# Performance work log

Measured on AMD Instinct MI355X. Metric: run time of the kernel, lower is better.

## Reference

```python
import jax, jax.numpy as jnp
import numpy as np
import math

B, L, H, U = 4, 4096, 1024, 1024


def setup_inputs() -> dict:
    key = jax.random.key(0)
    k_in, k_wi, k_bi, k_wo, k_bo, k_u = jax.random.split(key, 6)
    inputs = jax.random.normal(k_in, (B, L, H), dtype=jnp.float32)
    # Linear layers (torch Linear: y = x @ W.T + b), scaled like torch default init
    Wi = jax.random.normal(k_wi, (U, H), dtype=jnp.float32) / math.sqrt(H)
    bi = jax.random.normal(k_bi, (U,), dtype=jnp.float32) * 0.01
    Wo = jax.random.normal(k_wo, (H, U), dtype=jnp.float32) / math.sqrt(U)
    bo = jax.random.normal(k_bo, (H,), dtype=jnp.float32) * 0.01
    # LRU-style init of nu_log / gamma_log, exactly as in the torch __init__
    r_min, r_max = 0.9, 0.999
    u = jax.random.uniform(k_u, (U,), dtype=jnp.float32)
    nu_log = jnp.log(-0.5 * jnp.log(u * (r_max ** 2 - r_min ** 2) + r_min ** 2))
    gamma_log = jnp.log(jnp.sqrt(1.0 - jnp.exp(-jnp.exp(nu_log)) ** 2))
    params_log = jnp.stack([nu_log, gamma_log])  # [2, U]
    return {"inputs": inputs, "Wi": Wi, "bi": bi, "Wo": Wo, "bo": bo,
            "params_log": params_log}


def reference(inputs, Wi, bi, Wo, bo, params_log):
    # u = i_dense(inputs): [B, L, U]
    u = jnp.einsum('blh,uh->blu', inputs, Wi) + bi
    params = jnp.exp(params_log)
    nu, gamma = params[0], params[1]  # each [U]

    log2_L = int(np.ceil(np.log2(L)))
    pad_len = 2 ** log2_L - L
    x = jnp.pad(u, ((0, 0), (0, pad_len), (0, 0))) if pad_len else u
    Lp = 2 ** log2_L

    # Log-depth doubling parallel scan: h_t = exp(-nu) * h_{t-1} + u_t
    for i in range(1, log2_L + 1):
        l = 2 ** i
        x = x.reshape(B * Lp // l, l, U)
        x1, x2 = x[:, : l // 2], x[:, l // 2:]
        pos = jnp.arange(1, l // 2 + 1, dtype=jnp.float32)  # [l/2]
        lambs = jnp.exp(-pos[:, None] * nu)                  # [l/2, U]
        x2 = x2 + lambs * x1[:, -1:]
        x = jnp.concatenate([x1, x2], axis=1).reshape(B, Lp, U)

    x = x[:, :L] * gamma
    # o_dense: [B, L, H]
    return jnp.einsum('blu,hu->blh', x, Wo) + bo
```

## Files before the change

kernel.cpp:

```cpp
#include <hip/hip_runtime.h>

#define B_DIM 4
#define L_DIM 4096
#define H_DIM 1024
#define U_DIM 1024
#define M_DIM (B_DIM * L_DIM)
#define LC 64
#define NCH (L_DIM / LC)

using f32x4  = __attribute__((ext_vector_type(4))) float;
using bf16x8 = __attribute__((ext_vector_type(8))) __bf16;
using us8    = __attribute__((ext_vector_type(8))) unsigned short;
using u32x2  = __attribute__((ext_vector_type(2))) unsigned int;

__device__ inline unsigned short f32_to_bf16(float f) {
  unsigned int u = __float_as_uint(f);
  u += 0x7FFF + ((u >> 16) & 1);
  return (unsigned short)(u >> 16);
}
__device__ inline float bf16_to_f32(unsigned short v) {
  return __uint_as_float((unsigned int)v << 16);
}

__device__ inline void async_load16(const void* g, void* l) {
  __builtin_amdgcn_global_load_lds(
      (const __attribute__((address_space(1))) void*)g,
      (__attribute__((address_space(3))) void*)l, 16, 0, 0);
}

#define IN_ELEMS  (M_DIM * H_DIM)
#define WI_ELEMS  (U_DIM * H_DIM)
#define WO_ELEMS  (H_DIM * U_DIM)
#define CVT_TOTAL (IN_ELEMS + WI_ELEMS + WO_ELEMS)

__global__ __launch_bounds__(256) void cvt_all(
    const float* __restrict__ inp, const float* __restrict__ wi,
    const float* __restrict__ wo,
    unsigned short* __restrict__ inp_b, unsigned short* __restrict__ wi_b,
    unsigned short* __restrict__ wo_b)
{
  size_t e = ((size_t)blockIdx.x * 256 + threadIdx.x) * 8;
  if (e >= CVT_TOTAL) return;
  const float* src; unsigned short* dst; size_t off;
  if (e < IN_ELEMS)                 { src = inp; dst = inp_b; off = e; }
  else if (e < IN_ELEMS + WI_ELEMS) { src = wi;  dst = wi_b;  off = e - IN_ELEMS; }
  else                              { src = wo;  dst = wo_b;  off = e - IN_ELEMS - WI_ELEMS; }
  f32x4 a = *(const f32x4*)(src + off);
  f32x4 b = *(const f32x4*)(src + off + 4);
  us8 r;
  r[0] = f32_to_bf16(a.x); r[1] = f32_to_bf16(a.y);
  r[2] = f32_to_bf16(a.z); r[3] = f32_to_bf16(a.w);
  r[4] = f32_to_bf16(b.x); r[5] = f32_to_bf16(b.y);
  r[6] = f32_to_bf16(b.z); r[7] = f32_to_bf16(b.w);
  *(us8*)(dst + off) = r;
}

#define BM 256
#define BN 256
#define BK 64

template <typename OUT>
__global__ __launch_bounds__(512, 2) void gemm256(
    const unsigned short* __restrict__ A, const unsigned short* __restrict__ Bm,
    const float* __restrict__ bias, OUT* __restrict__ C,
    int M, int N, int K)
{
  __shared__ __attribute__((aligned(16))) char lds[131072];

  const int tid  = threadIdx.x;
  const int lane = tid & 63;
  const int wave = tid >> 6;
  const int wm   = wave >> 2;
  const int wn   = wave & 3;

  const int nby = M / BM;
  const int sby = nby >> 3;
  const int p   = blockIdx.x;
  const int xcd = p & 7;
  const int j   = p >> 3;
  const int by  = xcd * sby + (j % sby);
  const int bx  = j / sby;
  const int m0  = by * BM;
  const int n0  = bx * BN;

  const size_t rowb = (size_t)K * 2;
  const int NTk = K / BK;

  const int srow  = tid >> 3;
  const int scs16 = ((tid & 7) ^ (srow & 7)) << 4;
  const char* Ab = (const char*)A;
  const char* Bb = (const char*)Bm;

  auto stA = [&](int buf, int half, int kt) {
    const char* g = Ab + (size_t)(m0 + half * 128 + srow) * rowb + (size_t)kt * 128 + scs16;
    char* d = lds + buf * 65536 + half * 16384 + tid * 16;
    async_load16(g, d);
    async_load16(g + 64 * rowb, d + 8192);
  };
  auto stB = [&](int buf, int half, int kt) {
    const char* g = Bb + (size_t)(n0 + half * 128 + srow) * rowb + (size_t)kt * 128 + scs16;
    char* d = lds + buf * 65536 + 32768 + half * 16384 + tid * 16;
    async_load16(g, d);
    async_load16(g + 64 * rowb, d + 8192);
  };

  const int arow = wm * 128 + (lane & 15);
  const int brow = wn * 64  + (lane & 15);
  const int ch0  = (((lane >> 4)    ) ^ (lane & 7)) << 4;
  const int ch1  = (((lane >> 4) | 4) ^ (lane & 7)) << 4;

  f32x4 acc[8][4];
  #pragma unroll
  for (int i = 0; i < 8; ++i)
    #pragma unroll
    for (int q = 0; q < 4; ++q)
      acc[i][q] = {0.f, 0.f, 0.f, 0.f};

  stA(0, 0, 0); stA(0, 1, 0); stB(0, 0, 0); stB(0, 1, 0);
  stA(1, 0, 1); stA(1, 1, 1);
  asm volatile("s_waitcnt vmcnt(4)" ::: "memory");
  __builtin_amdgcn_sched_barrier(0);
  __builtin_amdgcn_s_barrier();

  for (int w = 0; w < NTk; ++w) {
    const int cur = w & 1;
    const char* pa = lds + cur * 65536 + arow * 128;
    const char* pb = lds + cur * 65536 + 32768 + brow * 128;
    bf16x8 af[8][2], bfr[4][2];

    #pragma unroll
    for (int mi = 0; mi < 4; ++mi) {
      af[mi][0] = *(const bf16x8*)(pa + mi * 2048 + ch0);
      af[mi][1] = *(const bf16x8*)(pa + mi * 2048 + ch1);
    }
    #pragma unroll
    for (int ni = 0; ni < 2; ++ni) {
      bfr[ni][0] = *(const bf16x8*)(pb + ni * 2048 + ch0);
      bfr[ni][1] = *(const bf16x8*)(pb + ni * 2048 + ch1);
    }
    if (w + 1 < NTk) stB(cur ^ 1, 0, w + 1);
    __builtin_amdgcn_s_barrier();
    asm volatile("s_waitcnt lgkmcnt(0)" ::: "memory");
    __builtin_amdgcn_sched_barrier(0);
    __builtin_amdgcn_s_setprio(1);
    #pragma unroll
    for (int mi = 0; mi < 4; ++mi)
      #pragma unroll
      for (int ni = 0; ni < 2; ++ni) {
        acc[mi][ni] = __builtin_amdgcn_mfma_f32_16x16x32_bf16(bfr[ni][0], af[mi][0], acc[mi][ni], 0, 0, 0);
        acc[mi][ni] = __builtin_amdgcn_mfma_f32_16x16x32_bf16(bfr[ni][1], af[mi][1], acc[mi][ni], 0, 0, 0);
      }
    __builtin_amdgcn_s_setprio(0);

    #pragma unroll
    for (int mi = 4; mi < 8; ++mi) {
      af[mi][0] = *(const bf16x8*)(pa + mi * 2048 + ch0);
      af[mi][1] = *(const bf16x8*)(pa + mi * 2048 + ch1);
    }
    if (w + 1 < NTk) stB(cur ^ 1, 1, w + 1);
    __builtin_amdgcn_s_barrier();
    asm volatile("s_waitcnt lgkmcnt(0)" ::: "memory");
    __builtin_amdgcn_sched_barrier(0);
    __builtin_amdgcn_s_setprio(1);
    #pragma unroll
    for (int mi = 4; mi < 8; ++mi)
      #pragma unroll
      for (int ni = 0; ni < 2; ++ni) {
        acc[mi][ni] = __builtin_amdgcn_mfma_f32_16x16x32_bf16(bfr[ni][0], af[mi][0], acc[mi][ni], 0, 0, 0);
        acc[mi][ni] = __builtin_amdgcn_mfma_f32_16x16x32_bf16(bfr[ni][1], af[mi][1], acc[mi][ni], 0, 0, 0);
      }
    __builtin_amdgcn_s_setprio(0);

    #pragma unroll
    for (int ni = 2; ni < 4; ++ni) {
      bfr[ni][0] = *(const bf16x8*)(pb + ni * 2048 + ch0);
      bfr[ni][1] = *(const bf16x8*)(pb + ni * 2048 + ch1);
    }
    __builtin_amdgcn_s_barrier();
    asm volatile("s_waitcnt lgkmcnt(0)" ::: "memory");
    __builtin_amdgcn_sched_barrier(0);
    __builtin_amdgcn_s_setprio(1);
    #pragma unroll
    for (int mi = 0; mi < 4; ++mi)
      #pragma unroll
      for (int ni = 2; ni < 4; ++ni) {
        acc[mi][ni] = __builtin_amdgcn_mfma_f32_16x16x32_bf16(bfr[ni][0], af[mi][0], acc[mi][ni], 0, 0, 0);
        acc[mi][ni] = __builtin_amdgcn_mfma_f32_16x16x32_bf16(bfr[ni][1], af[mi][1], acc[mi][ni], 0, 0, 0);
      }
    __builtin_amdgcn_s_setprio(0);

    if (w + 2 < NTk) { stA(cur, 0, w + 2); stA(cur, 1, w + 2); }
    if (w < NTk - 2) asm volatile("s_waitcnt vmcnt(4)" ::: "memory");
    else             asm volatile("s_waitcnt vmcnt(0)" ::: "memory");
    __builtin_amdgcn_sched_barrier(0);
    __builtin_amdgcn_s_barrier();
    __builtin_amdgcn_s_setprio(1);
    #pragma unroll
    for (int mi = 4; mi < 8; ++mi)
      #pragma unroll
      for (int ni = 2; ni < 4; ++ni) {
        acc[mi][ni] = __builtin_amdgcn_mfma_f32_16x16x32_bf16(bfr[ni][0], af[mi][0], acc[mi][ni], 0, 0, 0);
        acc[mi][ni] = __builtin_amdgcn_mfma_f32_16x16x32_bf16(bfr[ni][1], af[mi][1], acc[mi][ni], 0, 0, 0);
      }
    __builtin_amdgcn_s_setprio(0);
  }

  const int q4 = (lane >> 4) * 4;
  #pragma unroll
  for (int mi = 0; mi < 8; ++mi) {
    const int row = m0 + wm * 128 + mi * 16 + (lane & 15);
    #pragma unroll
    for (int ni = 0; ni < 4; ++ni) {
      const int ncol = n0 + wn * 64 + ni * 16 + q4;
      const f32x4 bv = *(const f32x4*)(bias + ncol);
      f32x4 v = acc[mi][ni];
      v.x += bv.x; v.y += bv.y; v.z += bv.z; v.w += bv.w;
      if constexpr (sizeof(OUT) == 2) {
        u32x2 pk;
        pk.x = ((unsigned)f32_to_bf16(v.y) << 16) | (unsigned)f32_to_bf16(v.x);
        pk.y = ((unsigned)f32_to_bf16(v.w) << 16) | (unsigned)f32_to_bf16(v.z);
        *(u32x2*)((unsigned short*)C + (size_t)row * N + ncol) = pk;
      } else {
        *(f32x4*)((float*)C + (size_t)row * N + ncol) = v;
      }
    }
  }
}

__global__ __launch_bounds__(256) void scan_carry(
    const unsigned short* __restrict__ u, const float* __restrict__ params_log,
    float* __restrict__ carry)
{
  int uu = blockIdx.x * 256 + threadIdx.x;
  int c  = blockIdx.y;
  int b  = blockIdx.z;
  float l = expf(-expf(params_log[uu]));
  const unsigned short* p = u + (size_t)(b * L_DIM + c * LC) * U_DIM + uu;
  float s = 0.f;
  #pragma unroll 8
  for (int j = 0; j < LC; ++j)
    s = fmaf(s, l, bf16_to_f32(p[(size_t)j * U_DIM]));
  carry[((size_t)b * NCH + c) * U_DIM + uu] = s;
}

__global__ __launch_bounds__(256) void scan_prefix(
    const float* __restrict__ carry, const float* __restrict__ params_log,
    float* __restrict__ prefix)
{
  int wid  = (blockIdx.x * 256 + threadIdx.x) >> 6;
  int lane = threadIdx.x & 63;
  int b  = wid >> 10;
  int uu = wid & (U_DIM - 1);
  float lp = expf(-expf(params_log[uu]) * (float)LC);
  const float* cp = carry + (size_t)b * NCH * U_DIM + uu;
  float s = cp[(size_t)lane * U_DIM];
  float a = lp;
  #pragma unroll
  for (int d = 1; d < 64; d <<= 1) {
    float s_up = __shfl_up(s, d, 64);
    float a_up = __shfl_up(a, d, 64);
    if (lane >= d) { s = fmaf(a, s_up, s); a *= a_up; }
  }
  float ex = __shfl_up(s, 1, 64);
  if (lane == 0) ex = 0.f;
  prefix[((size_t)b * NCH + lane) * U_DIM + uu] = ex;
}

__global__ __launch_bounds__(256) void scan_apply(
    const unsigned short* __restrict__ u, const float* __restrict__ params_log,
    const float* __restrict__ prefix, unsigned short* __restrict__ x_b)
{
  int uu = blockIdx.x * 256 + threadIdx.x;
  int c  = blockIdx.y;
  int b  = blockIdx.z;
  float l = expf(-expf(params_log[uu]));
  float g = expf(params_log[U_DIM + uu]);
  float s = prefix[((size_t)b * NCH + c) * U_DIM + uu];
  const unsigned short* p = u + (size_t)(b * L_DIM + c * LC) * U_DIM + uu;
  unsigned short* q = x_b + (size_t)(b * L_DIM + c * LC) * U_DIM + uu;
  #pragma unroll 8
  for (int j = 0; j < LC; ++j) {
    s = fmaf(s, l, bf16_to_f32(p[(size_t)j * U_DIM]));
    q[(size_t)j * U_DIM] = f32_to_bf16(s * g);
  }
}

extern "C" void kernel_launch(void* const* d_in, const int* in_sizes, int n_in,
                              void* d_out, int out_size, void* d_ws, size_t ws_size,
                              hipStream_t stream)
{
  const float* inputs     = (const float*)d_in[0];
  const float* Wi         = (const float*)d_in[1];
  const float* bi         = (const float*)d_in[2];
  const float* Wo         = (const float*)d_in[3];
  const float* bo         = (const float*)d_in[4];
  const float* params_log = (const float*)d_in[5];
  float* out = (float*)d_out;

  char* ws = (char*)d_ws;
  unsigned short* u_b    = (unsigned short*)(ws);
  unsigned short* x_b    = (unsigned short*)(ws + (32u << 20));
  unsigned short* in_b   = (unsigned short*)(ws + (64u << 20));
  unsigned short* wi_b   = (unsigned short*)(ws + (96u << 20));
  unsigned short* wo_b   = (unsigned short*)(ws + (98u << 20));
  float*          carry  = (float*)(ws + (100u << 20));
  float*          prefix = (float*)(ws + (101u << 20));

  cvt_all<<<dim3((CVT_TOTAL / 8 + 255) / 256), 256, 0, stream>>>(
      inputs, Wi, Wo, in_b, wi_b, wo_b);

  gemm256<unsigned short><<<dim3((M_DIM / BM) * (U_DIM / BN)), 512, 0, stream>>>(
      in_b, wi_b, bi, u_b, M_DIM, U_DIM, H_DIM);

  scan_carry <<<dim3(U_DIM / 256, NCH, B_DIM), 256, 0, stream>>>(u_b, params_log, carry);
  scan_prefix<<<dim3(B_DIM * U_DIM * 64 / 256), 256, 0, stream>>>(carry, params_log, prefix);
  scan_apply <<<dim3(U_DIM / 256, NCH, B_DIM), 256, 0, stream>>>(u_b, params_log, prefix, x_b);

  gemm256<float><<<dim3((M_DIM / BM) * (H_DIM / BN)), 512, 0, stream>>>(
      x_b, wo_b, bo, out, M_DIM, H_DIM, U_DIM);
}
```

Before: 227.3 us.

## Fuse fp32-to-bf16 input conversion into first GEMM's A-tile loads

Drops the separate conversion pass over the large fp32 input tensor. The first GEMM now reads fp32 A tiles into registers, converts them to bf16, and writes them to LDS with the same swizzle, prefetching two k-steps ahead. This removes a full read plus a bf16 write and re-read of the input. In exchange, A tiles now go through registers with a full vmcnt(0) wait each iteration, which adds register pressure and weakens overlap compared with the async LDS loads. Each GEMM tile also re-reads A at twice the byte size across the N blocks.

```diff
diff --git a/kernel.cpp b/kernel.cpp
--- a/kernel.cpp
+++ b/kernel.cpp
@@ -28,23 +28,19 @@
       (__attribute__((address_space(3))) void*)l, 16, 0, 0);
 }
 
-#define IN_ELEMS  (M_DIM * H_DIM)
 #define WI_ELEMS  (U_DIM * H_DIM)
 #define WO_ELEMS  (H_DIM * U_DIM)
-#define CVT_TOTAL (IN_ELEMS + WI_ELEMS + WO_ELEMS)
-
-__global__ __launch_bounds__(256) void cvt_all(
-    const float* __restrict__ inp, const float* __restrict__ wi,
-    const float* __restrict__ wo,
-    unsigned short* __restrict__ inp_b, unsigned short* __restrict__ wi_b,
-    unsigned short* __restrict__ wo_b)
+#define CVT2_TOTAL (WI_ELEMS + WO_ELEMS)
+
+__global__ __launch_bounds__(256) void cvt_w(
+    const float* __restrict__ wi, const float* __restrict__ wo,
+    unsigned short* __restrict__ wi_b, unsigned short* __restrict__ wo_b)
 {
   size_t e = ((size_t)blockIdx.x * 256 + threadIdx.x) * 8;
-  if (e >= CVT_TOTAL) return;
+  if (e >= CVT2_TOTAL) return;
   const float* src; unsigned short* dst; size_t off;
-  if (e < IN_ELEMS)                 { src = inp; dst = inp_b; off = e; }
-  else if (e < IN_ELEMS + WI_ELEMS) { src = wi;  dst = wi_b;  off = e - IN_ELEMS; }
-  else                              { src = wo;  dst = wo_b;  off = e - IN_ELEMS - WI_ELEMS; }
+  if (e < WI_ELEMS) { src = wi; dst = wi_b; off = e; }
+  else              { src = wo; dst = wo_b; off = e - WI_ELEMS; }
   f32x4 a = *(const f32x4*)(src + off);
   f32x4 b = *(const f32x4*)(src + off + 4);
   us8 r;
@@ -59,9 +55,9 @@
 #define BN 256
 #define BK 64
 
-template <typename OUT>
+template <typename OUT, bool A32>
 __global__ __launch_bounds__(512, 2) void gemm256(
-    const unsigned short* __restrict__ A, const unsigned short* __restrict__ Bm,
+    const void* __restrict__ Av, const unsigned short* __restrict__ Bm,
     const float* __restrict__ bias, OUT* __restrict__ C,
     int M, int N, int K)
 {
@@ -83,16 +79,18 @@
   const int m0  = by * BM;
   const int n0  = bx * BN;
 
-  const size_t rowb = (size_t)K * 2;
   const int NTk = K / BK;
 
   const int srow  = tid >> 3;
   const int scs16 = ((tid & 7) ^ (srow & 7)) << 4;
-  const char* Ab = (const char*)A;
+  const int cs8   = ((tid & 7) ^ (srow & 7)) << 3;
+  const unsigned short* Ab16 = (const unsigned short*)Av;
+  const float*          Af   = (const float*)Av;
   const char* Bb = (const char*)Bm;
+  const size_t rowb = (size_t)K * 2;
 
   auto stA = [&](int buf, int half, int kt) {
-    const char* g = Ab + (size_t)(m0 + half * 128 + srow) * rowb + (size_t)kt * 128 + scs16;
+    const char* g = (const char*)Ab16 + (size_t)(m0 + half * 128 + srow) * rowb + (size_t)kt * 128 + scs16;
     char* d = lds + buf * 65536 + half * 16384 + tid * 16;
     async_load16(g, d);
     async_load16(g + 64 * rowb, d + 8192);
@@ -103,6 +101,26 @@
     async_load16(g, d);
     async_load16(g + 64 * rowb, d + 8192);
   };
+  auto aldA = [&](f32x4 t[4][2], int kt) {
+    #pragma unroll
+    for (int idx = 0; idx < 4; ++idx) {
+      const float* g = Af + (size_t)(m0 + (idx >> 1) * 128 + (idx & 1) * 64 + srow) * K
+                         + (size_t)kt * 64 + cs8;
+      t[idx][0] = *(const f32x4*)g;
+      t[idx][1] = *(const f32x4*)(g + 4);
+    }
+  };
+  auto awrA = [&](f32x4 t[4][2], int buf) {
+    #pragma unroll
+    for (int idx = 0; idx < 4; ++idx) {
+      us8 pk;
+      pk[0] = f32_to_bf16(t[idx][0].x); pk[1] = f32_to_bf16(t[idx][0].y);
+      pk[2] = f32_to_bf16(t[idx][0].z); pk[3] = f32_to_bf16(t[idx][0].w);
+      pk[4] = f32_to_bf16(t[idx][1].x); pk[5] = f32_to_bf16(t[idx][1].y);
+      pk[6] = f32_to_bf16(t[idx][1].z); pk[7] = f32_to_bf16(t[idx][1].w);
+      *(us8*)(lds + buf * 65536 + (idx >> 1) * 16384 + (idx & 1) * 8192 + tid * 16) = pk;
+    }
+  };
 
   const int arow = wm * 128 + (lane & 15);
   const int brow = wn * 64  + (lane & 15);
@@ -116,17 +134,32 @@
     for (int q = 0; q < 4; ++q)
       acc[i][q] = {0.f, 0.f, 0.f, 0.f};
 
-  stA(0, 0, 0); stA(0, 1, 0); stB(0, 0, 0); stB(0, 1, 0);
-  stA(1, 0, 1); stA(1, 1, 1);
-  asm volatile("s_waitcnt vmcnt(4)" ::: "memory");
-  __builtin_amdgcn_sched_barrier(0);
-  __builtin_amdgcn_s_barrier();
+  if constexpr (A32) {
+    f32x4 t0[4][2], t1[4][2];
+    aldA(t0, 0);
+    stB(0, 0, 0); stB(0, 1, 0);
+    aldA(t1, 1);
+    asm volatile("s_waitcnt vmcnt(12)" ::: "memory");
+    awrA(t0, 0);
+    asm volatile("s_waitcnt vmcnt(0)" ::: "memory");
+    awrA(t1, 1);
+    asm volatile("s_waitcnt lgkmcnt(0)" ::: "memory");
+    __builtin_amdgcn_sched_barrier(0);
+    __builtin_amdgcn_s_barrier();
+  } else {
+    stA(0, 0, 0); stA(0, 1, 0); stB(0, 0, 0); stB(0, 1, 0);
+    stA(1, 0, 1); stA(1, 1, 1);
+    asm volatile("s_waitcnt vmcnt(4)" ::: "memory");
+    __builtin_amdgcn_sched_barrier(0);
+    __builtin_amdgcn_s_barrier();
+  }
 
   for (int w = 0; w < NTk; ++w) {
     const int cur = w & 1;
     const char* pa = lds + cur * 65536 + arow * 128;
     const char* pb = lds + cur * 65536 + 32768 + brow * 128;
     bf16x8 af[8][2], bfr[4][2];
+    f32x4 areg[4][2];
 
     #pragma unroll
     for (int mi = 0; mi < 4; ++mi) {
@@ -138,6 +171,7 @@
       bfr[ni][0] = *(const bf16x8*)(pb + ni * 2048 + ch0);
       bfr[ni][1] = *(const bf16x8*)(pb + ni * 2048 + ch1);
     }
+    if constexpr (A32) { if (w + 2 < NTk) aldA(areg, w + 2); }
     if (w + 1 < NTk) stB(cur ^ 1, 0, w + 1);
     __builtin_amdgcn_s_barrier();
     asm volatile("s_waitcnt lgkmcnt(0)" ::: "memory");
@@ -189,9 +223,14 @@
       }
     __builtin_amdgcn_s_setprio(0);
 
-    if (w + 2 < NTk) { stA(cur, 0, w + 2); stA(cur, 1, w + 2); }
-    if (w < NTk - 2) asm volatile("s_waitcnt vmcnt(4)" ::: "memory");
-    else             asm volatile("s_waitcnt vmcnt(0)" ::: "memory");
+    if constexpr (A32) {
+      asm volatile("s_waitcnt vmcnt(0)" ::: "memory");
+      if (w + 2 < NTk) awrA(areg, cur);
+    } else {
+      if (w + 2 < NTk) { stA(cur, 0, w + 2); stA(cur, 1, w + 2); }
+      if (w < NTk - 2) asm volatile("s_waitcnt vmcnt(4)" ::: "memory");
+      else             asm volatile("s_waitcnt vmcnt(0)" ::: "memory");
+    }
     __builtin_amdgcn_sched_barrier(0);
     __builtin_amdgcn_s_barrier();
     __builtin_amdgcn_s_setprio(1);
@@ -300,22 +339,20 @@
   char* ws = (char*)d_ws;
   unsigned short* u_b    = (unsigned short*)(ws);
   unsigned short* x_b    = (unsigned short*)(ws + (32u << 20));
-  unsigned short* in_b   = (unsigned short*)(ws + (64u << 20));
   unsigned short* wi_b   = (unsigned short*)(ws + (96u << 20));
   unsigned short* wo_b   = (unsigned short*)(ws + (98u << 20));
   float*          carry  = (float*)(ws + (100u << 20));
   float*          prefix = (float*)(ws + (101u << 20));
 
-  cvt_all<<<dim3((CVT_TOTAL / 8 + 255) / 256), 256, 0, stream>>>(
-      inputs, Wi, Wo, in_b, wi_b, wo_b);
-
-  gemm256<unsigned short><<<dim3((M_DIM / BM) * (U_DIM / BN)), 512, 0, stream>>>(
-      in_b, wi_b, bi, u_b, M_DIM, U_DIM, H_DIM);
+  cvt_w<<<dim3((CVT2_TOTAL / 8 + 255) / 256), 256, 0, stream>>>(Wi, Wo, wi_b, wo_b);
+
+  gemm256<unsigned short, true><<<dim3((M_DIM / BM) * (U_DIM / BN)), 512, 0, stream>>>(
+      inputs, wi_b, bi, u_b, M_DIM, U_DIM, H_DIM);
 
   scan_carry <<<dim3(U_DIM / 256, NCH, B_DIM), 256, 0, stream>>>(u_b, params_log, carry);
   scan_prefix<<<dim3(B_DIM * U_DIM * 64 / 256), 256, 0, stream>>>(carry, params_log, prefix);
   scan_apply <<<dim3(U_DIM / 256, NCH, B_DIM), 256, 0, stream>>>(u_b, params_log, prefix, x_b);
 
-  gemm256<float><<<dim3((M_DIM / BM) * (H_DIM / BN)), 512, 0, stream>>>(
+  gemm256<float, false><<<dim3((M_DIM / BM) * (H_DIM / BN)), 512, 0, stream>>>(
       x_b, wo_b, bo, out, M_DIM, H_DIM, U_DIM);
 }
```

Result: slower. 255.9 us (+12.6%).

## Vectorize scan kernels to 8 channels per thread and fuse prefix into apply

Applied to the files above, without the earlier changes.

Each scan thread now handles eight adjacent channels with 16-byte loads and stores instead of one 2-byte element, so memory accesses are wider. The separate shuffle-based prefix kernel is removed. Each apply thread instead serially folds the carries of all preceding chunks before running its own chunk, which drops one launch and the prefix buffer. The cost is redundant serial work that grows with chunk index (up to 63 steps) and far fewer threads per launch (128 blocks), which may reduce latency hiding.

```diff
diff --git a/kernel.cpp b/kernel.cpp
--- a/kernel.cpp
+++ b/kernel.cpp
@@ -231,57 +231,74 @@
     const unsigned short* __restrict__ u, const float* __restrict__ params_log,
     float* __restrict__ carry)
 {
-  int uu = blockIdx.x * 256 + threadIdx.x;
-  int c  = blockIdx.y;
-  int b  = blockIdx.z;
-  float l = expf(-expf(params_log[uu]));
-  const unsigned short* p = u + (size_t)(b * L_DIM + c * LC) * U_DIM + uu;
-  float s = 0.f;
-  #pragma unroll 8
-  for (int j = 0; j < LC; ++j)
-    s = fmaf(s, l, bf16_to_f32(p[(size_t)j * U_DIM]));
-  carry[((size_t)b * NCH + c) * U_DIM + uu] = s;
-}
-
-__global__ __launch_bounds__(256) void scan_prefix(
-    const float* __restrict__ carry, const float* __restrict__ params_log,
-    float* __restrict__ prefix)
-{
-  int wid  = (blockIdx.x * 256 + threadIdx.x) >> 6;
-  int lane = threadIdx.x & 63;
-  int b  = wid >> 10;
-  int uu = wid & (U_DIM - 1);
-  float lp = expf(-expf(params_log[uu]) * (float)LC);
-  const float* cp = carry + (size_t)b * NCH * U_DIM + uu;
-  float s = cp[(size_t)lane * U_DIM];
-  float a = lp;
+  const int u0 = (threadIdx.x & 127) * 8;
+  const int c  = blockIdx.x * 2 + (threadIdx.x >> 7);
+  const int b  = blockIdx.y;
+  f32x4 n0 = *(const f32x4*)(params_log + u0);
+  f32x4 n1 = *(const f32x4*)(params_log + u0 + 4);
+  float l[8], s[8];
   #pragma unroll
-  for (int d = 1; d < 64; d <<= 1) {
-    float s_up = __shfl_up(s, d, 64);
-    float a_up = __shfl_up(a, d, 64);
-    if (lane >= d) { s = fmaf(a, s_up, s); a *= a_up; }
-  }
-  float ex = __shfl_up(s, 1, 64);
-  if (lane == 0) ex = 0.f;
-  prefix[((size_t)b * NCH + lane) * U_DIM + uu] = ex;
-}
-
-__global__ __launch_bounds__(256) void scan_apply(
-    const unsigned short* __restrict__ u, const float* __restrict__ params_log,
-    const float* __restrict__ prefix, unsigned short* __restrict__ x_b)
-{
-  int uu = blockIdx.x * 256 + threadIdx.x;
-  int c  = blockIdx.y;
-  int b  = blockIdx.z;
-  float l = expf(-expf(params_log[uu]));
-  float g = expf(params_log[U_DIM + uu]);
-  float s = prefix[((size_t)b * NCH + c) * U_DIM + uu];
-  const unsigned short* p = u + (size_t)(b * L_DIM + c * LC) * U_DIM + uu;
-  unsigned short* q = x_b + (size_t)(b * L_DIM + c * LC) * U_DIM + uu;
+  for (int i = 0; i < 8; ++i) {
+    float nv = (i < 4) ? n0[i] : n1[i - 4];
+    l[i] = expf(-expf(nv));
+    s[i] = 0.f;
+  }
+  const unsigned short* p = u + (size_t)(b * L_DIM + c * LC) * U_DIM + u0;
   #pragma unroll 8
   for (int j = 0; j < LC; ++j) {
-    s = fmaf(s, l, bf16_to_f32(p[(size_t)j * U_DIM]));
-    q[(size_t)j * U_DIM] = f32_to_bf16(s * g);
+    us8 v = *(const us8*)(p + (size_t)j * U_DIM);
+    #pragma unroll
+    for (int i = 0; i < 8; ++i)
+      s[i] = fmaf(s[i], l[i], bf16_to_f32(v[i]));
+  }
+  float* cp = carry + ((size_t)b * NCH + c) * U_DIM + u0;
+  f32x4 o0 = {s[0], s[1], s[2], s[3]};
+  f32x4 o1 = {s[4], s[5], s[6], s[7]};
+  *(f32x4*)cp = o0;
+  *(f32x4*)(cp + 4) = o1;
+}
+
+__global__ __launch_bounds__(256) void scan_papply(
+    const unsigned short* __restrict__ u, const float* __restrict__ params_log,
+    const float* __restrict__ carry, unsigned short* __restrict__ x_b)
+{
+  const int u0 = (threadIdx.x & 127) * 8;
+  const int c  = blockIdx.x * 2 + (threadIdx.x >> 7);
+  const int b  = blockIdx.y;
+  f32x4 n0 = *(const f32x4*)(params_log + u0);
+  f32x4 n1 = *(const f32x4*)(params_log + u0 + 4);
+  f32x4 g0 = *(const f32x4*)(params_log + U_DIM + u0);
+  f32x4 g1 = *(const f32x4*)(params_log + U_DIM + u0 + 4);
+  float l[8], lp[8], g[8], s[8];
+  #pragma unroll
+  for (int i = 0; i < 8; ++i) {
+    float nv = (i < 4) ? n0[i] : n1[i - 4];
+    float e  = expf(nv);
+    l[i]  = expf(-e);
+    lp[i] = expf(-e * (float)LC);
+    g[i]  = expf((i < 4) ? g0[i] : g1[i - 4]);
+    s[i]  = 0.f;
+  }
+  const float* cp = carry + (size_t)b * NCH * U_DIM + u0;
+  for (int cc = 0; cc < c; ++cc) {
+    f32x4 v0 = *(const f32x4*)(cp + (size_t)cc * U_DIM);
+    f32x4 v1 = *(const f32x4*)(cp + (size_t)cc * U_DIM + 4);
+    #pragma unroll
+    for (int i = 0; i < 8; ++i)
+      s[i] = fmaf(s[i], lp[i], (i < 4) ? v0[i] : v1[i - 4]);
+  }
+  const unsigned short* p = u + (size_t)(b * L_DIM + c * LC) * U_DIM + u0;
+  unsigned short* q = x_b + (size_t)(b * L_DIM + c * LC) * U_DIM + u0;
+  #pragma unroll 4
+  for (int j = 0; j < LC; ++j) {
+    us8 v = *(const us8*)(p + (size_t)j * U_DIM);
+    us8 o;
+    #pragma unroll
+    for (int i = 0; i < 8; ++i) {
+      s[i] = fmaf(s[i], l[i], bf16_to_f32(v[i]));
+      o[i] = f32_to_bf16(s[i] * g[i]);
+    }
+    *(us8*)(q + (size_t)j * U_DIM) = o;
   }
 }
 
@@ -304,7 +321,6 @@
   unsigned short* wi_b   = (unsigned short*)(ws + (96u << 20));
   unsigned short* wo_b   = (unsigned short*)(ws + (98u << 20));
   float*          carry  = (float*)(ws + (100u << 20));
-  float*          prefix = (float*)(ws + (101u << 20));
 
   cvt_all<<<dim3((CVT_TOTAL / 8 + 255) / 256), 256, 0, stream>>>(
       inputs, Wi, Wo, in_b, wi_b, wo_b);
@@ -312,9 +328,8 @@
   gemm256<unsigned short><<<dim3((M_DIM / BM) * (U_DIM / BN)), 512, 0, stream>>>(
       in_b, wi_b, bi, u_b, M_DIM, U_DIM, H_DIM);
 
-  scan_carry <<<dim3(U_DIM / 256, NCH, B_DIM), 256, 0, stream>>>(u_b, params_log, carry);
-  scan_prefix<<<dim3(B_DIM * U_DIM * 64 / 256), 256, 0, stream>>>(carry, params_log, prefix);
-  scan_apply <<<dim3(U_DIM / 256, NCH, B_DIM), 256, 0, stream>>>(u_b, params_log, prefix, x_b);
+  scan_carry <<<dim3(NCH / 2, B_DIM), 256, 0, stream>>>(u_b, params_log, carry);
+  scan_papply<<<dim3(NCH / 2, B_DIM), 256, 0, stream>>>(u_b, params_log, carry, x_b);
 
   gemm256<float><<<dim3((M_DIM / BM) * (H_DIM / BN)), 512, 0, stream>>>(
       x_b, wo_b, bo, out, M_DIM, H_DIM, U_DIM);
```

Result: slower. 238.6 us (+5.0%).
